# Performance work log

Hardware: AMD Instinct MI355X
Metric: run time of the kernel (lower is better)

The kernel has to match this reference:

```python
import jax, jax.numpy as jnp
import numpy as np

N, E, F_IN, H, T, OUT, ATTR = 20000, 640000, 128, 128, 12, 64, 4


def _glorot(key, shape):
    lim = 1.0 / np.sqrt(shape[0])
    return jax.random.uniform(key, shape, jnp.float32, -lim, lim)


def setup_inputs() -> dict:
    key = jax.random.key(0)
    ks = jax.random.split(key, 48)
    inp = {
        "x": jax.random.normal(ks[0], (N, F_IN, T), jnp.float32),
        "edge_attr": jax.random.uniform(ks[1], (E, ATTR), jnp.float32),
        "edge_index": jax.random.randint(ks[2], (2, E), 0, N, jnp.int32),
    }
    k = 3
    for i, cin in enumerate([F_IN, H]):
        gi = cin + 2 * H
        inp[f"gw{i}"] = _glorot(ks[k], (cin, H)); k += 1
        inp[f"gb{i}"] = jnp.zeros((H,), jnp.float32)
        for g in ["f", "i", "o", "c"]:
            inp[f"w{g}{i}"] = _glorot(ks[k], (gi, H)); k += 1
            inp[f"b{g}{i}"] = jnp.zeros((H,), jnp.float32)
    inp["ow"] = _glorot(ks[k], (H, OUT)); k += 1
    inp["ob"] = jnp.zeros((OUT,), jnp.float32)
    return inp


def _forward(edge_index, x, edge_attr, gw0, gb0, wf0, bf0, wi0, bi0, wo0, bo0, wc0, bc0,
             gw1, gb1, wf1, bf1, wi1, bi1, wo1, bo1, wc1, bc1, ow, ob):
    n = x.shape[0]
    ew = edge_attr[:, -1]
    row, col = edge_index[0], edge_index[1]
    # GCN normalization with self-loops (PyG gcn_norm, improved=False)
    sl = jnp.arange(n, dtype=row.dtype)
    r = jnp.concatenate([row, sl])
    c = jnp.concatenate([col, sl])
    w = jnp.concatenate([ew, jnp.ones((n,), ew.dtype)])
    deg = jax.ops.segment_sum(w, c, num_segments=n)
    dis = jnp.where(deg > 0, 1.0, 0.0) * jax.lax.rsqrt(jnp.where(deg > 0, deg, 1.0))
    norm = dis[r] * w * dis[c]  # [E+N]

    params = [(gw0, gb0, wf0, bf0, wi0, bi0, wo0, bo0, wc0, bc0),
              (gw1, gb1, wf1, bf1, wi1, bi1, wo1, bo1, wc1, bc1)]

    def gcn(xt, gw, gb):
        xw = xt @ gw  # [N,H]
        return jax.ops.segment_sum(norm[:, None] * xw[r], c, num_segments=n) + gb

    def cell(xt, h, cc, p):
        gw, gb, wf, bf, wi, bi, wo, bo, wc, bc = p
        g = jax.nn.sigmoid(gcn(xt, gw, gb))
        zu = jnp.concatenate([xt, g, h], axis=-1)  # [N, in+2H]
        f_t = jax.nn.sigmoid(zu @ wf + bf)
        i_t = jax.nn.sigmoid(zu @ wi + bi)
        o_t = jax.nn.sigmoid(zu @ wo + bo)
        c_t = jnp.tanh(zu @ wc + bc)
        cn = f_t * cc + i_t * c_t
        hn = o_t * jnp.tanh(cn)
        return hn, cn

    z = jnp.zeros((n, H), x.dtype)

    def step(carry, xt):
        inp_t = xt
        new = []
        for i2, p in enumerate(params):
            h, cc = cell(inp_t, carry[i2][0], carry[i2][1], p)
            new.append((h, cc))
            inp_t = h
        return tuple(new), None

    xs = jnp.transpose(x, (2, 0, 1))  # [T, N, F]
    carry, _ = jax.lax.scan(step, tuple((z, z) for _ in params), xs)
    return carry[-1][0] @ ow + ob  # output_activation = Identity


def reference(x, edge_attr, edge_index, gw0, gb0, wf0, bf0, wi0, bi0, wo0, bo0, wc0, bc0,
              gw1, gb1, wf1, bf1, wi1, bi1, wo1, bo1, wc1, bc1, ow, ob):
    return _forward(edge_index, x, edge_attr, gw0, gb0, wf0, bf0, wi0, bi0, wo0, bo0, wc0, bc0,
                    gw1, gb1, wf1, bf1, wi1, bi1, wo1, bo1, wc1, bc1, ow, ob)
```

## Files before the change

kernel.cpp:

```cpp
#include <hip/hip_runtime.h>
#include <hip/hip_bf16.h>

typedef unsigned short u16;
typedef unsigned int   u32;
typedef __attribute__((ext_vector_type(8))) short bf16x8;
typedef __attribute__((ext_vector_type(4))) float f32x4;

#define HDIM 128
#define TSTEPS 12
#define OUTD 64

#define AS1 __attribute__((address_space(1)))
#define AS3 __attribute__((address_space(3)))

__device__ __forceinline__ void glds16(const void* g, void* l) {
  __builtin_amdgcn_global_load_lds((const AS1 u32*)g, (AS3 u32*)l, 16, 0, 0);
}

__device__ __forceinline__ float bflo(u32 u) { return __uint_as_float(u << 16); }
__device__ __forceinline__ float bfhi(u32 u) { return __uint_as_float(u & 0xffff0000u); }
__device__ __forceinline__ u16 f2bf(float x) {
  union { float f; u32 u; } v; v.f = x;
  return (u16)((v.u + 0x7fffu + ((v.u >> 16) & 1u)) >> 16);
}
__device__ __forceinline__ float sigm(float x) { return 1.0f / (1.0f + __expf(-x)); }
__device__ __forceinline__ float tanh_f(float x) { return 1.0f - 2.0f / (__expf(2.0f * x) + 1.0f); }


__global__ void k_init(float* c0, float* c1, u16* h0z, u16* h1z, int* cnt, int* cursor, int N) {
  int i = blockIdx.x * 256 + threadIdx.x;
  int nh = N * HDIM;
  if (i < nh) { c0[i] = 0.f; c1[i] = 0.f; h0z[i] = 0; h1z[i] = 0; }
  if (i < N) { cnt[i] = 1; cursor[i] = 0; }
}

__global__ void k_xpose(const float* __restrict__ x, u16* __restrict__ xb, int N) {
  int i = blockIdx.x * 256 + threadIdx.x;
  if (i >= N * HDIM) return;
  const float* src = x + (size_t)i * 12;
  float4 a = *(const float4*)src;
  float4 b = *(const float4*)(src + 4);
  float4 c = *(const float4*)(src + 8);
  float v[12] = { a.x,a.y,a.z,a.w,b.x,b.y,b.z,b.w,c.x,c.y,c.z,c.w };
#pragma unroll
  for (int t = 0; t < 12; ++t) xb[(size_t)t * N * HDIM + i] = f2bf(v[t]);
}

__global__ void k_cnt(const int* __restrict__ ei, int* cnt, int E) {
  int e = blockIdx.x * 256 + threadIdx.x;
  if (e >= E) return;
  atomicAdd(&cnt[ei[E + e]], 1);
}

__global__ void k_scan(const int* __restrict__ cnt, int* __restrict__ rp, int n) {
  __shared__ int sums[1024];
  int tid = threadIdx.x;
  int chunk = (n + 1023) / 1024;
  int start = tid * chunk;
  int end = start + chunk; if (end > n) end = n;
  int s = 0;
  for (int i = start; i < end; ++i) s += cnt[i];
  sums[tid] = s;
  __syncthreads();
  for (int off = 1; off < 1024; off <<= 1) {
    int v = (tid >= off) ? sums[tid - off] : 0;
    __syncthreads();
    sums[tid] += v;
    __syncthreads();
  }
  int run = (tid == 0) ? 0 : sums[tid - 1];
  for (int i = start; i < end; ++i) { rp[i] = run; run += cnt[i]; }
  if (tid == 1023) rp[n] = sums[1023];
}

__global__ void k_scatter(const int* __restrict__ ei, const float* __restrict__ ea,
                          const int* __restrict__ rp, int* cursor, uint2* ee, int E) {
  int e = blockIdx.x * 256 + threadIdx.x;
  if (e >= E) return;
  int row = ei[e], col = ei[E + e];
  int pos = atomicAdd(&cursor[col], 1);
  int idx = rp[col] + 1 + pos;
  ee[idx] = make_uint2((u32)row << 8, __float_as_uint(ea[e * 4 + 3]));
}

__global__ void k_degcsr(const int* __restrict__ rp, uint2* ee, float* dis, int N) {
  int j = blockIdx.x;
  int lane = threadIdx.x;
  int beg = rp[j], end = rp[j + 1];
  float s = 0.f;
  for (int i = beg + 1 + lane; i < end; i += 64) s += __uint_as_float(ee[i].y);
#pragma unroll
  for (int o = 32; o; o >>= 1) s += __shfl_down(s, o);
  if (lane == 0) {
    dis[j] = rsqrtf(1.0f + s);
    ee[beg] = make_uint2((u32)j << 8, __float_as_uint(1.0f));
  }
}

__global__ void k_enrm(const int* __restrict__ rp, const float* __restrict__ dis,
                       uint2* ee, int N) {
  int j = blockIdx.x;
  int lane = threadIdx.x;
  int beg = rp[j], end = rp[j + 1];
  float dj = dis[j];
  for (int i = beg + lane; i < end; i += 64) {
    uint2 q = ee[i];
    ee[i].y = __float_as_uint(dis[q.x >> 8] * __uint_as_float(q.y) * dj);
  }
}

__global__ void k_wt(const float* __restrict__ src, u16* __restrict__ dst, int K, int J, int ldK) {
  int idx = blockIdx.x * 256 + threadIdx.x;
  if (idx >= K * J) return;
  int k = idx / J, j = idx % J;
  dst[j * ldK + k] = f2bf(src[idx]);
}

__global__ void k_wt4(const float* wf, const float* wi, const float* wo, const float* wc,
                      u16* __restrict__ dst) {
  int idx = blockIdx.x * 256 + threadIdx.x;
  if (idx >= 512 * 384) return;
  int p = idx / 384, k = idx % 384;
  int g = (p >> 4) & 3;
  int hc = (p & 15) | ((p >> 6) << 4);
  const float* w[4] = { wf, wi, wo, wc };
  dst[p * 384 + k] = f2bf(w[g][k * HDIM + hc]);
}

__global__ void k_bias4(const float* bf, const float* bi, const float* bo, const float* bc,
                        float* dst) {
  int p = blockIdx.x * 256 + threadIdx.x;
  if (p >= 512) return;
  int g = (p >> 4) & 3;
  int hc = (p & 15) | ((p >> 6) << 4);
  const float* b[4] = { bf, bi, bo, bc };
  dst[p] = b[g][hc];
}

struct GA {
  const u16* s0; const u16* s1; const u16* s2;
  const u16* wt;
  const float* b4; float* cst; u16* hout;
};
struct GJ { const u16* A; const u16* wt; u16* out; };

__global__ __launch_bounds__(256)
void k_mega(GA ga0, GA ga1, GJ gj, int gjM, int ngate, int M) {
  __shared__ u16 lA[128 * 32];
  __shared__ u16 lB[128 * 32];
  const int y = blockIdx.y;
  const int tid = threadIdx.x;
  const int row0 = blockIdx.x * 128;
  const int wave = tid >> 6, lane = tid & 63;
  const int wm = (wave >> 1) * 64, wn = (wave & 1) * 64;
  const int fr = lane & 15, fk = (lane >> 4) * 8;
  const int lr = tid >> 2, lc = (tid & 3) * 8;
  u16* ldA = lA + wave * 512;
  u16* ldB = lB + wave * 512;
  f32x4 acc[4][4] = {};
  const int fq4 = (lane >> 4) * 4;

  if (y < 4 * ngate) {
    const GA& ga = (y < 4) ? ga0 : ga1;
    const int yy = y & 3;
    const int col0 = yy * 128;
    const u16* segs[3] = { ga.s0, ga.s1, ga.s2 };
    const u16* gb1 = ga.wt + (size_t)(col0 + lr) * 384 + lc;
    const u16* gb2 = gb1 + (size_t)64 * 384;
    const size_t arow1 = (size_t)(row0 + lr) * HDIM + lc;
    const size_t arow2 = arow1 + (size_t)64 * HDIM;

    for (int ks = 0; ks < 12; ++ks) {
      const int k0 = ks * 32;
      const u16* As = segs[ks >> 2];
      const int kk = k0 & 127;
      glds16(As + arow1 + kk, ldA);
      glds16(As + arow2 + kk, ldA + 2048);
      glds16(gb1 + k0, ldB);
      glds16(gb2 + k0, ldB + 2048);
      __syncthreads();
      bf16x8 af[4], bfx[4];
#pragma unroll
      for (int m = 0; m < 4; ++m) af[m]  = *(const bf16x8*)&lA[(wm + m * 16 + fr) * 32 + fk];
#pragma unroll
      for (int n = 0; n < 4; ++n) bfx[n] = *(const bf16x8*)&lB[(wn + n * 16 + fr) * 32 + fk];
#pragma unroll
      for (int m = 0; m < 4; ++m)
#pragma unroll
        for (int n = 0; n < 4; ++n)
          acc[m][n] = __builtin_amdgcn_mfma_f32_16x16x32_bf16(af[m], bfx[n], acc[m][n], 0, 0, 0);
      __syncthreads();
    }

    const int hc = fr | ((yy * 2 + (wave & 1)) << 4);
    const int colbase = col0 + wn + fr;
    const float bb0 = ga.b4[colbase];
    const float bb1 = ga.b4[colbase + 16];
    const float bb2 = ga.b4[colbase + 32];
    const float bb3 = ga.b4[colbase + 48];
#pragma unroll
    for (int m = 0; m < 4; ++m)
#pragma unroll
      for (int i = 0; i < 4; ++i) {
        const int rowg = row0 + wm + m * 16 + fq4 + i;
        if (rowg < M) {
          float f_ = sigm(acc[m][0][i] + bb0);
          float i_ = sigm(acc[m][1][i] + bb1);
          float o_ = sigm(acc[m][2][i] + bb2);
          float cd = tanh_f(acc[m][3][i] + bb3);
          size_t idx = (size_t)rowg * HDIM + hc;
          float cn = f_ * ga.cst[idx] + i_ * cd;
          ga.cst[idx] = cn;
          ga.hout[idx] = f2bf(o_ * tanh_f(cn));
        }
      }
  } else {
    if (row0 >= gjM) return;
    const u16* ga1p = gj.A + (size_t)(row0 + lr) * HDIM + lc;
    const u16* ga2p = ga1p + (size_t)64 * HDIM;
    const u16* gb1p = gj.wt + (size_t)lr * HDIM + lc;
    const u16* gb2p = gb1p + (size_t)64 * HDIM;
    for (int k0 = 0; k0 < 128; k0 += 32) {
      glds16(ga1p + k0, ldA);
      glds16(ga2p + k0, ldA + 2048);
      glds16(gb1p + k0, ldB);
      glds16(gb2p + k0, ldB + 2048);
      __syncthreads();
      bf16x8 af[4], bfx[4];
#pragma unroll
      for (int m = 0; m < 4; ++m) af[m]  = *(const bf16x8*)&lA[(wm + m * 16 + fr) * 32 + fk];
#pragma unroll
      for (int n = 0; n < 4; ++n) bfx[n] = *(const bf16x8*)&lB[(wn + n * 16 + fr) * 32 + fk];
#pragma unroll
      for (int m = 0; m < 4; ++m)
#pragma unroll
        for (int n = 0; n < 4; ++n)
          acc[m][n] = __builtin_amdgcn_mfma_f32_16x16x32_bf16(af[m], bfx[n], acc[m][n], 0, 0, 0);
      __syncthreads();
    }
#pragma unroll
    for (int m = 0; m < 4; ++m)
#pragma unroll
      for (int n = 0; n < 4; ++n) {
        const int colg = wn + n * 16 + fr;
#pragma unroll
        for (int i = 0; i < 4; ++i) {
          const int rowg = row0 + wm + m * 16 + fq4 + i;
          if (rowg < gjM) gj.out[(size_t)rowg * HDIM + colg] = f2bf(acc[m][n][i]);
        }
      }
  }
}

__global__ void k_agg(const u16* __restrict__ xw, const int* __restrict__ rp,
                      const uint2* __restrict__ ee, const float* __restrict__ gb,
                      u16* __restrict__ g, int N) {
  __shared__ uint2 s_e[64];
  const char* xwb = (const char*)xw;
  int bid = blockIdx.x;
  int j = bid % N;
  u32 tbase = (u32)(bid - j) << 8;
  int lane = threadIdx.x;
  int beg = rp[j], end = rp[j + 1];
  const int sl = lane & 31, half = lane >> 5;
  const u32 slB = (u32)sl * 8;
  float a0 = 0.f, a1 = 0.f, a2 = 0.f, a3 = 0.f;
  for (int cb = beg; cb < end; cb += 64) {
    int mc = end - cb; if (mc > 64) mc = 64;
    uint2 q;
    if (lane < mc) { q = ee[cb + lane]; q.x += tbase; }
    else { q.x = tbase; q.y = 0u; }
    s_e[lane] = q;
    __syncthreads();
    int np = (mc + 1) >> 1;
    for (int p = 0; p < np; ++p) {
      uint2 r = s_e[p * 2 + half];
      float w = __uint_as_float(r.y);
      uint2 v = *(const uint2*)(xwb + (r.x + slB));
      a0 += w * bflo(v.x);
      a1 += w * bfhi(v.x);
      a2 += w * bflo(v.y);
      a3 += w * bfhi(v.y);
    }
    __syncthreads();
  }
  a0 += __shfl_xor(a0, 32);
  a1 += __shfl_xor(a1, 32);
  a2 += __shfl_xor(a2, 32);
  a3 += __shfl_xor(a3, 32);
  if (half == 0) {
    float4 bv = *(const float4*)(gb + sl * 4);
    a0 = sigm(a0 + bv.x); a1 = sigm(a1 + bv.y);
    a2 = sigm(a2 + bv.z); a3 = sigm(a3 + bv.w);
    uint2 o;
    o.x = ((u32)f2bf(a1) << 16) | (u32)f2bf(a0);
    o.y = ((u32)f2bf(a3) << 16) | (u32)f2bf(a2);
    *(uint2*)((char*)g + (((size_t)bid) << 8) + slB) = o;
  }
}

__global__ void k_out(const u16* __restrict__ h, const float* __restrict__ ow,
                      const float* __restrict__ ob, float* __restrict__ out, int M) {
  __shared__ float lw[HDIM * OUTD];
  __shared__ float lb[OUTD];
  int tid = threadIdx.x;
  for (int i = tid; i < HDIM * OUTD; i += 256) lw[i] = ow[i];
  if (tid < OUTD) lb[tid] = ob[tid];
  __syncthreads();
  int j = tid & 63;
  int nl = tid >> 6;
  int n = blockIdx.x * 4 + nl;
  if (n >= M) return;
  const u16* hr = h + (size_t)n * HDIM;
  float s = lb[j];
#pragma unroll 4
  for (int k = 0; k < HDIM; ++k) s += bflo((u32)hr[k] << 0 ? (u32)hr[k] : (u32)hr[k]) * 0.f + __uint_as_float(((u32)hr[k]) << 16) * lw[k * OUTD + j];
  out[(size_t)n * OUTD + j] = s;
}

extern "C" void kernel_launch(void* const* d_in, const int* in_sizes, int n_in,
                              void* d_out, int out_size, void* d_ws, size_t ws_size,
                              hipStream_t stream) {
  const float* x  = (const float*)d_in[0];
  const float* ea = (const float*)d_in[1];
  const int*   ei = (const int*)d_in[2];
  const float* gw[2] = { (const float*)d_in[3],  (const float*)d_in[13] };
  const float* gb[2] = { (const float*)d_in[4],  (const float*)d_in[14] };
  const float* wg[2][4] = {
    { (const float*)d_in[5],  (const float*)d_in[7],  (const float*)d_in[9],  (const float*)d_in[11] },
    { (const float*)d_in[15], (const float*)d_in[17], (const float*)d_in[19], (const float*)d_in[21] } };
  const float* bg[2][4] = {
    { (const float*)d_in[6],  (const float*)d_in[8],  (const float*)d_in[10], (const float*)d_in[12] },
    { (const float*)d_in[16], (const float*)d_in[18], (const float*)d_in[20], (const float*)d_in[22] } };
  const float* ow = (const float*)d_in[23];
  const float* ob = (const float*)d_in[24];
  float* out = (float*)d_out;

  const int N = in_sizes[0] / (HDIM * TSTEPS);
  const int E = in_sizes[2] / 2;
  const int nh = N * HDIM;
  const int tnh = TSTEPS * nh;

  size_t off = 0;
  auto alloc = [&](size_t bytes) -> void* {
    void* p = (char*)d_ws + off;
    off += (bytes + 255) & ~(size_t)255;
    return p;
  };
  u16* xb     = (u16*)alloc((size_t)tnh * 2);
  u16* xw_all = (u16*)alloc((size_t)tnh * 2);
  u16* g0_all = (u16*)alloc((size_t)tnh * 2);
  u16* H0[3] = { (u16*)alloc((size_t)nh * 2), (u16*)alloc((size_t)nh * 2), (u16*)alloc((size_t)nh * 2) };
  u16* H1[2] = { (u16*)alloc((size_t)nh * 2), (u16*)alloc((size_t)nh * 2) };
  u16* g1buf = (u16*)alloc((size_t)nh * 2);
  u16* xw1[2] = { (u16*)alloc((size_t)nh * 2), (u16*)alloc((size_t)nh * 2) };
  float* cst[2] = { (float*)alloc((size_t)nh * 4), (float*)alloc((size_t)nh * 4) };
  float* dis   = (float*)alloc((size_t)N * 4);
  int* cnt     = (int*)alloc((size_t)N * 4);
  int* cursor  = (int*)alloc((size_t)N * 4);
  int* rp      = (int*)alloc((size_t)(N + 1) * 4);
  uint2* ee    = (uint2*)alloc((size_t)(E + N) * 8);
  u16* gwT[2] = { (u16*)alloc(HDIM * HDIM * 2), (u16*)alloc(HDIM * HDIM * 2) };
  u16* w4T[2] = { (u16*)alloc(512 * 384 * 2),   (u16*)alloc(512 * 384 * 2) };
  float* b4[2] = { (float*)alloc(512 * 4), (float*)alloc(512 * 4) };
  alloc(32768);

  k_init<<<(nh + 255) / 256, 256, 0, stream>>>(cst[0], cst[1], H0[2], H1[1], cnt, cursor, N);
  k_xpose<<<(nh + 255) / 256, 256, 0, stream>>>(x, xb, N);
  k_cnt<<<(E + 255) / 256, 256, 0, stream>>>(ei, cnt, E);
  k_scan<<<1, 1024, 0, stream>>>(cnt, rp, N);
  k_scatter<<<(E + 255) / 256, 256, 0, stream>>>(ei, ea, rp, cursor, ee, E);
  k_degcsr<<<N, 64, 0, stream>>>(rp, ee, dis, N);
  k_enrm<<<N, 64, 0, stream>>>(rp, dis, ee, N);
  for (int l = 0; l < 2; ++l) {
    k_wt<<<(HDIM * HDIM + 255) / 256, 256, 0, stream>>>(gw[l], gwT[l], HDIM, HDIM, HDIM);
    k_wt4<<<(512 * 384 + 255) / 256, 256, 0, stream>>>(wg[l][0], wg[l][1], wg[l][2], wg[l][3], w4T[l]);
    k_bias4<<<2, 256, 0, stream>>>(bg[l][0], bg[l][1], bg[l][2], bg[l][3], b4[l]);
  }

  const int nb = (N + 127) / 128;
  GA zga = { xb, xb, xb, w4T[0], b4[0], cst[0], H0[0] };
  GJ zgj = { xb, gwT[0], xw_all };

  {
    int Mb = tnh / HDIM;
    GJ gj = { xb, gwT[0], xw_all };
    k_mega<<<dim3((Mb + 127) / 128, 1), 256, 0, stream>>>(zga, zga, gj, Mb, 0, N);
  }
  k_agg<<<TSTEPS * N, 64, 0, stream>>>(xw_all, rp, ee, gb[0], g0_all, N);

  {
    GA a0 = { xb, g0_all, H0[2], w4T[0], b4[0], cst[0], H0[0] };
    k_mega<<<dim3(nb, 4), 256, 0, stream>>>(a0, a0, zgj, N, 1, N);
  }
  {
    GA a0 = { xb + (size_t)nh, g0_all + (size_t)nh, H0[0], w4T[0], b4[0], cst[0], H0[1] };
    GJ gj = { H0[0], gwT[1], xw1[0] };
    k_mega<<<dim3(nb, 5), 256, 0, stream>>>(a0, a0, gj, N, 1, N);
  }

  for (int t = 0; t < TSTEPS; ++t) {
    k_agg<<<N, 64, 0, stream>>>(xw1[t & 1], rp, ee, gb[1], g1buf, N);
    GA a0 = { H0[t % 3], g1buf, H1[(t + 1) & 1], w4T[1], b4[1], cst[1], H1[t & 1] };
    int ngate = 1, hasg = 0;
    GA a1 = a0;
    GJ gj = zgj;
    if (t + 2 < TSTEPS) {
      a1 = GA{ xb + (size_t)(t + 2) * nh, g0_all + (size_t)(t + 2) * nh, H0[(t + 1) % 3],
               w4T[0], b4[0], cst[0], H0[(t + 2) % 3] };
      ngate = 2;
    }
    if (t + 1 < TSTEPS) {
      gj = GJ{ H0[(t + 1) % 3], gwT[1], xw1[(t + 1) & 1] };
      hasg = 1;
    }
    k_mega<<<dim3(nb, 4 * ngate + hasg), 256, 0, stream>>>(a0, a1, gj, N, ngate, N);
  }
  k_out<<<(N + 3) / 4, 256, 0, stream>>>(H1[1], ow, ob, out, N);
}
```

Baseline: 1.439 ms.

## Run layers sequentially with node-major all-timestep GCN aggregation

Restructures the schedule so that layer 0 runs for all timesteps first, then layer 1. Each layer's GCN linear step and neighbour aggregation now run once over all 12 timesteps, using a node-major layout so one CSR traversal per node gathers every timestep's features in a single contiguous row. This replaces the per-step aggregation launches for layer 1 and the fused mega-kernel with separate gate kernels. It removes the repeated edge-list traversals and many small launches. In exchange it keeps all layer-0 hidden states in memory, reuses buffers, and drops the overlap of layer-0 and layer-1 work within a single launch.

```diff
diff --git a/kernel.cpp b/kernel.cpp
--- a/kernel.cpp
+++ b/kernel.cpp
@@ -9,9 +9,13 @@
 #define HDIM 128
 #define TSTEPS 12
 #define OUTD 64
+#define NTMAJ 1536
+#define NTB   3072
 
 #define AS1 __attribute__((address_space(1)))
 #define AS3 __attribute__((address_space(3)))
+
+struct u32x3 { u32 x, y, z; };
 
 __device__ __forceinline__ void glds16(const void* g, void* l) {
   __builtin_amdgcn_global_load_lds((const AS1 u32*)g, (AS3 u32*)l, 16, 0, 0);
@@ -27,11 +31,14 @@
 __device__ __forceinline__ float tanh_f(float x) { return 1.0f - 2.0f / (__expf(2.0f * x) + 1.0f); }
 
 
-__global__ void k_init(float* c0, float* c1, u16* h0z, u16* h1z, int* cnt, int* cursor, int N) {
+__global__ void k_init(int* cnt, int* cursor, int N) {
   int i = blockIdx.x * 256 + threadIdx.x;
-  int nh = N * HDIM;
-  if (i < nh) { c0[i] = 0.f; c1[i] = 0.f; h0z[i] = 0; h1z[i] = 0; }
   if (i < N) { cnt[i] = 1; cursor[i] = 0; }
+}
+
+__global__ void k_zero(u32* p, int n) {
+  int i = blockIdx.x * 256 + threadIdx.x;
+  if (i < n) p[i] = 0;
 }
 
 __global__ void k_xpose(const float* __restrict__ x, u16* __restrict__ xb, int N) {
@@ -80,7 +87,7 @@
   int row = ei[e], col = ei[E + e];
   int pos = atomicAdd(&cursor[col], 1);
   int idx = rp[col] + 1 + pos;
-  ee[idx] = make_uint2((u32)row << 8, __float_as_uint(ea[e * 4 + 3]));
+  ee[idx] = make_uint2((u32)row * NTB, __float_as_uint(ea[e * 4 + 3]));
 }
 
 __global__ void k_degcsr(const int* __restrict__ rp, uint2* ee, float* dis, int N) {
@@ -93,7 +100,7 @@
   for (int o = 32; o; o >>= 1) s += __shfl_down(s, o);
   if (lane == 0) {
     dis[j] = rsqrtf(1.0f + s);
-    ee[beg] = make_uint2((u32)j << 8, __float_as_uint(1.0f));
+    ee[beg] = make_uint2((u32)j * NTB, __float_as_uint(1.0f));
   }
 }
 
@@ -105,7 +112,7 @@
   float dj = dis[j];
   for (int i = beg + lane; i < end; i += 64) {
     uint2 q = ee[i];
-    ee[i].y = __float_as_uint(dis[q.x >> 8] * __uint_as_float(q.y) * dj);
+    ee[i].y = __float_as_uint(dis[q.x / NTB] * __uint_as_float(q.y) * dj);
   }
 }
 
@@ -137,18 +144,12 @@
   dst[p] = b[g][hc];
 }
 
-struct GA {
-  const u16* s0; const u16* s1; const u16* s2;
-  const u16* wt;
-  const float* b4; float* cst; u16* hout;
-};
-struct GJ { const u16* A; const u16* wt; u16* out; };
-
 __global__ __launch_bounds__(256)
-void k_mega(GA ga0, GA ga1, GJ gj, int gjM, int ngate, int M) {
+void k_gcnlin(const u16* __restrict__ A, const u16* __restrict__ wt,
+              u16* __restrict__ out, int N, int nh) {
   __shared__ u16 lA[128 * 32];
   __shared__ u16 lB[128 * 32];
-  const int y = blockIdx.y;
+  const int t = blockIdx.y;
   const int tid = threadIdx.x;
   const int row0 = blockIdx.x * 128;
   const int wave = tid >> 6, lane = tid & 63;
@@ -157,146 +158,154 @@
   const int lr = tid >> 2, lc = (tid & 3) * 8;
   u16* ldA = lA + wave * 512;
   u16* ldB = lB + wave * 512;
+  const u16* ga1 = A + (size_t)t * nh + (size_t)(row0 + lr) * HDIM + lc;
+  const u16* ga2 = ga1 + (size_t)64 * HDIM;
+  const u16* gb1 = wt + (size_t)lr * HDIM + lc;
+  const u16* gb2 = gb1 + (size_t)64 * HDIM;
+
   f32x4 acc[4][4] = {};
+  for (int k0 = 0; k0 < 128; k0 += 32) {
+    glds16(ga1 + k0, ldA);
+    glds16(ga2 + k0, ldA + 2048);
+    glds16(gb1 + k0, ldB);
+    glds16(gb2 + k0, ldB + 2048);
+    __syncthreads();
+    bf16x8 af[4], bfx[4];
+#pragma unroll
+    for (int m = 0; m < 4; ++m) af[m]  = *(const bf16x8*)&lA[(wm + m * 16 + fr) * 32 + fk];
+#pragma unroll
+    for (int n = 0; n < 4; ++n) bfx[n] = *(const bf16x8*)&lB[(wn + n * 16 + fr) * 32 + fk];
+#pragma unroll
+    for (int m = 0; m < 4; ++m)
+#pragma unroll
+      for (int n = 0; n < 4; ++n)
+        acc[m][n] = __builtin_amdgcn_mfma_f32_16x16x32_bf16(af[m], bfx[n], acc[m][n], 0, 0, 0);
+    __syncthreads();
+  }
   const int fq4 = (lane >> 4) * 4;
-
-  if (y < 4 * ngate) {
-    const GA& ga = (y < 4) ? ga0 : ga1;
-    const int yy = y & 3;
-    const int col0 = yy * 128;
-    const u16* segs[3] = { ga.s0, ga.s1, ga.s2 };
-    const u16* gb1 = ga.wt + (size_t)(col0 + lr) * 384 + lc;
-    const u16* gb2 = gb1 + (size_t)64 * 384;
-    const size_t arow1 = (size_t)(row0 + lr) * HDIM + lc;
-    const size_t arow2 = arow1 + (size_t)64 * HDIM;
-
-    for (int ks = 0; ks < 12; ++ks) {
-      const int k0 = ks * 32;
-      const u16* As = segs[ks >> 2];
-      const int kk = k0 & 127;
-      glds16(As + arow1 + kk, ldA);
-      glds16(As + arow2 + kk, ldA + 2048);
-      glds16(gb1 + k0, ldB);
-      glds16(gb2 + k0, ldB + 2048);
-      __syncthreads();
-      bf16x8 af[4], bfx[4];
-#pragma unroll
-      for (int m = 0; m < 4; ++m) af[m]  = *(const bf16x8*)&lA[(wm + m * 16 + fr) * 32 + fk];
-#pragma unroll
-      for (int n = 0; n < 4; ++n) bfx[n] = *(const bf16x8*)&lB[(wn + n * 16 + fr) * 32 + fk];
-#pragma unroll
-      for (int m = 0; m < 4; ++m)
-#pragma unroll
-        for (int n = 0; n < 4; ++n)
-          acc[m][n] = __builtin_amdgcn_mfma_f32_16x16x32_bf16(af[m], bfx[n], acc[m][n], 0, 0, 0);
-      __syncthreads();
-    }
-
-    const int hc = fr | ((yy * 2 + (wave & 1)) << 4);
-    const int colbase = col0 + wn + fr;
-    const float bb0 = ga.b4[colbase];
-    const float bb1 = ga.b4[colbase + 16];
-    const float bb2 = ga.b4[colbase + 32];
-    const float bb3 = ga.b4[colbase + 48];
-#pragma unroll
-    for (int m = 0; m < 4; ++m)
+#pragma unroll
+  for (int m = 0; m < 4; ++m)
+#pragma unroll
+    for (int n = 0; n < 4; ++n) {
+      const int colg = wn + n * 16 + fr;
 #pragma unroll
       for (int i = 0; i < 4; ++i) {
         const int rowg = row0 + wm + m * 16 + fq4 + i;
-        if (rowg < M) {
-          float f_ = sigm(acc[m][0][i] + bb0);
-          float i_ = sigm(acc[m][1][i] + bb1);
-          float o_ = sigm(acc[m][2][i] + bb2);
-          float cd = tanh_f(acc[m][3][i] + bb3);
-          size_t idx = (size_t)rowg * HDIM + hc;
-          float cn = f_ * ga.cst[idx] + i_ * cd;
-          ga.cst[idx] = cn;
-          ga.hout[idx] = f2bf(o_ * tanh_f(cn));
-        }
+        if (rowg < N) out[(size_t)rowg * NTMAJ + t * HDIM + colg] = f2bf(acc[m][n][i]);
       }
-  } else {
-    if (row0 >= gjM) return;
-    const u16* ga1p = gj.A + (size_t)(row0 + lr) * HDIM + lc;
-    const u16* ga2p = ga1p + (size_t)64 * HDIM;
-    const u16* gb1p = gj.wt + (size_t)lr * HDIM + lc;
-    const u16* gb2p = gb1p + (size_t)64 * HDIM;
-    for (int k0 = 0; k0 < 128; k0 += 32) {
-      glds16(ga1p + k0, ldA);
-      glds16(ga2p + k0, ldA + 2048);
-      glds16(gb1p + k0, ldB);
-      glds16(gb2p + k0, ldB + 2048);
-      __syncthreads();
-      bf16x8 af[4], bfx[4];
-#pragma unroll
-      for (int m = 0; m < 4; ++m) af[m]  = *(const bf16x8*)&lA[(wm + m * 16 + fr) * 32 + fk];
-#pragma unroll
-      for (int n = 0; n < 4; ++n) bfx[n] = *(const bf16x8*)&lB[(wn + n * 16 + fr) * 32 + fk];
-#pragma unroll
-      for (int m = 0; m < 4; ++m)
-#pragma unroll
-        for (int n = 0; n < 4; ++n)
-          acc[m][n] = __builtin_amdgcn_mfma_f32_16x16x32_bf16(af[m], bfx[n], acc[m][n], 0, 0, 0);
-      __syncthreads();
     }
+}
+
+__global__ __launch_bounds__(256)
+void k_gate3(const u16* __restrict__ p0, u32 st0,
+             const u16* __restrict__ p1, u32 st1,
+             const u16* __restrict__ p2, u32 st2,
+             const u16* __restrict__ wt, const float* __restrict__ b4p,
+             float* __restrict__ cst, u16* __restrict__ hout, int M) {
+  __shared__ u16 lA[128 * 32];
+  __shared__ u16 lB[128 * 32];
+  const int col0 = blockIdx.y * 128;
+  const int tid = threadIdx.x;
+  const int row0 = blockIdx.x * 128;
+  const int wave = tid >> 6, lane = tid & 63;
+  const int wm = (wave >> 1) * 64, wn = (wave & 1) * 64;
+  const int fr = lane & 15, fk = (lane >> 4) * 8;
+  const int lr = tid >> 2, lc = (tid & 3) * 8;
+  u16* ldA = lA + wave * 512;
+  u16* ldB = lB + wave * 512;
+  const u16* a1[3]; const u16* a2[3];
+  a1[0] = p0 + (size_t)(row0 + lr) * st0 + lc;  a2[0] = a1[0] + (size_t)64 * st0;
+  a1[1] = p1 + (size_t)(row0 + lr) * st1 + lc;  a2[1] = a1[1] + (size_t)64 * st1;
+  a1[2] = p2 + (size_t)(row0 + lr) * st2 + lc;  a2[2] = a1[2] + (size_t)64 * st2;
+  const u16* gb1 = wt + (size_t)(col0 + lr) * 384 + lc;
+  const u16* gb2 = gb1 + (size_t)64 * 384;
+
+  f32x4 acc[4][4] = {};
+#pragma unroll
+  for (int ks = 0; ks < 12; ++ks) {
+    const int seg = ks >> 2;
+    const int kk = (ks & 3) * 32;
+    glds16(a1[seg] + kk, ldA);
+    glds16(a2[seg] + kk, ldA + 2048);
+    glds16(gb1 + ks * 32, ldB);
+    glds16(gb2 + ks * 32, ldB + 2048);
+    __syncthreads();
+    bf16x8 af[4], bfx[4];
+#pragma unroll
+    for (int m = 0; m < 4; ++m) af[m]  = *(const bf16x8*)&lA[(wm + m * 16 + fr) * 32 + fk];
+#pragma unroll
+    for (int n = 0; n < 4; ++n) bfx[n] = *(const bf16x8*)&lB[(wn + n * 16 + fr) * 32 + fk];
 #pragma unroll
     for (int m = 0; m < 4; ++m)
 #pragma unroll
-      for (int n = 0; n < 4; ++n) {
-        const int colg = wn + n * 16 + fr;
-#pragma unroll
-        for (int i = 0; i < 4; ++i) {
-          const int rowg = row0 + wm + m * 16 + fq4 + i;
-          if (rowg < gjM) gj.out[(size_t)rowg * HDIM + colg] = f2bf(acc[m][n][i]);
-        }
+      for (int n = 0; n < 4; ++n)
+        acc[m][n] = __builtin_amdgcn_mfma_f32_16x16x32_bf16(af[m], bfx[n], acc[m][n], 0, 0, 0);
+    __syncthreads();
+  }
+
+  const int fq4 = (lane >> 4) * 4;
+  const int hc = fr | ((blockIdx.y * 2 + (wave & 1)) << 4);
+  const int colbase = col0 + wn + fr;
+  const float bb0 = b4p[colbase];
+  const float bb1 = b4p[colbase + 16];
+  const float bb2 = b4p[colbase + 32];
+  const float bb3 = b4p[colbase + 48];
+#pragma unroll
+  for (int m = 0; m < 4; ++m)
+#pragma unroll
+    for (int i = 0; i < 4; ++i) {
+      const int rowg = row0 + wm + m * 16 + fq4 + i;
+      if (rowg < M) {
+        float f_ = sigm(acc[m][0][i] + bb0);
+        float i_ = sigm(acc[m][1][i] + bb1);
+        float o_ = sigm(acc[m][2][i] + bb2);
+        float cd = tanh_f(acc[m][3][i] + bb3);
+        size_t idx = (size_t)rowg * HDIM + hc;
+        float cn = f_ * cst[idx] + i_ * cd;
+        cst[idx] = cn;
+        hout[idx] = f2bf(o_ * tanh_f(cn));
       }
-  }
-}
-
-__global__ void k_agg(const u16* __restrict__ xw, const int* __restrict__ rp,
-                      const uint2* __restrict__ ee, const float* __restrict__ gb,
-                      u16* __restrict__ g, int N) {
-  __shared__ uint2 s_e[64];
-  const char* xwb = (const char*)xw;
-  int bid = blockIdx.x;
-  int j = bid % N;
-  u32 tbase = (u32)(bid - j) << 8;
-  int lane = threadIdx.x;
-  int beg = rp[j], end = rp[j + 1];
-  const int sl = lane & 31, half = lane >> 5;
-  const u32 slB = (u32)sl * 8;
-  float a0 = 0.f, a1 = 0.f, a2 = 0.f, a3 = 0.f;
-  for (int cb = beg; cb < end; cb += 64) {
-    int mc = end - cb; if (mc > 64) mc = 64;
-    uint2 q;
-    if (lane < mc) { q = ee[cb + lane]; q.x += tbase; }
-    else { q.x = tbase; q.y = 0u; }
-    s_e[lane] = q;
-    __syncthreads();
-    int np = (mc + 1) >> 1;
-    for (int p = 0; p < np; ++p) {
-      uint2 r = s_e[p * 2 + half];
+    }
+}
+
+__global__ void k_aggB(const u16* __restrict__ xw, const int* __restrict__ rp,
+                       const uint2* __restrict__ ee, const float* __restrict__ gbias,
+                       u16* __restrict__ g, int N) {
+  __shared__ uint2 s_e[256];
+  __shared__ float s_b[128];
+  const int j = blockIdx.x;
+  const int tid = threadIdx.x;
+  if (tid < 128) s_b[tid] = gbias[tid];
+  const int beg = rp[j], end = rp[j + 1];
+  const char* base = (const char*)xw;
+  const u32 myoff = (u32)tid * 12;
+  float a0 = 0.f, a1 = 0.f, a2 = 0.f, a3 = 0.f, a4 = 0.f, a5 = 0.f;
+  for (int cb = beg; cb < end; cb += 256) {
+    int mc = end - cb; if (mc > 256) mc = 256;
+    if (tid < mc) s_e[tid] = ee[cb + tid];
+    __syncthreads();
+    for (int e = 0; e < mc; ++e) {
+      uint2 r = s_e[e];
       float w = __uint_as_float(r.y);
-      uint2 v = *(const uint2*)(xwb + (r.x + slB));
-      a0 += w * bflo(v.x);
-      a1 += w * bfhi(v.x);
-      a2 += w * bflo(v.y);
-      a3 += w * bfhi(v.y);
+      u32x3 v = *(const u32x3*)(base + (r.x + myoff));
+      a0 += w * bflo(v.x); a1 += w * bfhi(v.x);
+      a2 += w * bflo(v.y); a3 += w * bfhi(v.y);
+      a4 += w * bflo(v.z); a5 += w * bfhi(v.z);
     }
     __syncthreads();
   }
-  a0 += __shfl_xor(a0, 32);
-  a1 += __shfl_xor(a1, 32);
-  a2 += __shfl_xor(a2, 32);
-  a3 += __shfl_xor(a3, 32);
-  if (half == 0) {
-    float4 bv = *(const float4*)(gb + sl * 4);
-    a0 = sigm(a0 + bv.x); a1 = sigm(a1 + bv.y);
-    a2 = sigm(a2 + bv.z); a3 = sigm(a3 + bv.w);
-    uint2 o;
-    o.x = ((u32)f2bf(a1) << 16) | (u32)f2bf(a0);
-    o.y = ((u32)f2bf(a3) << 16) | (u32)f2bf(a2);
-    *(uint2*)((char*)g + (((size_t)bid) << 8) + slB) = o;
-  }
+  const int e0 = tid * 6;
+  float r0 = sigm(a0 + s_b[e0 & 127]);
+  float r1 = sigm(a1 + s_b[(e0 + 1) & 127]);
+  float r2 = sigm(a2 + s_b[(e0 + 2) & 127]);
+  float r3 = sigm(a3 + s_b[(e0 + 3) & 127]);
+  float r4 = sigm(a4 + s_b[(e0 + 4) & 127]);
+  float r5 = sigm(a5 + s_b[(e0 + 5) & 127]);
+  u32x3 o;
+  o.x = ((u32)f2bf(r1) << 16) | (u32)f2bf(r0);
+  o.y = ((u32)f2bf(r3) << 16) | (u32)f2bf(r2);
+  o.z = ((u32)f2bf(r5) << 16) | (u32)f2bf(r4);
+  *(u32x3*)((char*)g + ((size_t)j * NTB + myoff)) = o;
 }
 
 __global__ void k_out(const u16* __restrict__ h, const float* __restrict__ ow,
@@ -314,7 +323,7 @@
   const u16* hr = h + (size_t)n * HDIM;
   float s = lb[j];
 #pragma unroll 4
-  for (int k = 0; k < HDIM; ++k) s += bflo((u32)hr[k] << 0 ? (u32)hr[k] : (u32)hr[k]) * 0.f + __uint_as_float(((u32)hr[k]) << 16) * lw[k * OUTD + j];
+  for (int k = 0; k < HDIM; ++k) s += __uint_as_float(((u32)hr[k]) << 16) * lw[k * OUTD + j];
   out[(size_t)n * OUTD + j] = s;
 }
 
@@ -348,24 +357,24 @@
     return p;
   };
   u16* xb     = (u16*)alloc((size_t)tnh * 2);
-  u16* xw_all = (u16*)alloc((size_t)tnh * 2);
-  u16* g0_all = (u16*)alloc((size_t)tnh * 2);
-  u16* H0[3] = { (u16*)alloc((size_t)nh * 2), (u16*)alloc((size_t)nh * 2), (u16*)alloc((size_t)nh * 2) };
-  u16* H1[2] = { (u16*)alloc((size_t)nh * 2), (u16*)alloc((size_t)nh * 2) };
-  u16* g1buf = (u16*)alloc((size_t)nh * 2);
-  u16* xw1[2] = { (u16*)alloc((size_t)nh * 2), (u16*)alloc((size_t)nh * 2) };
-  float* cst[2] = { (float*)alloc((size_t)nh * 4), (float*)alloc((size_t)nh * 4) };
-  float* dis   = (float*)alloc((size_t)N * 4);
-  int* cnt     = (int*)alloc((size_t)N * 4);
-  int* cursor  = (int*)alloc((size_t)N * 4);
-  int* rp      = (int*)alloc((size_t)(N + 1) * 4);
-  uint2* ee    = (uint2*)alloc((size_t)(E + N) * 8);
+  u16* g_nm   = (u16*)alloc((size_t)tnh * 2);
+  u16* h0_all = (u16*)alloc((size_t)(TSTEPS + 1) * nh * 2);
+  float* cst  = (float*)alloc((size_t)nh * 4);
+  uint2* ee   = (uint2*)alloc((size_t)(E + N) * 8);
+  float* dis  = (float*)alloc((size_t)N * 4);
+  int* cnt    = (int*)alloc((size_t)N * 4);
+  int* cursor = (int*)alloc((size_t)N * 4);
+  int* rp     = (int*)alloc((size_t)(N + 1) * 4);
   u16* gwT[2] = { (u16*)alloc(HDIM * HDIM * 2), (u16*)alloc(HDIM * HDIM * 2) };
   u16* w4T[2] = { (u16*)alloc(512 * 384 * 2),   (u16*)alloc(512 * 384 * 2) };
   float* b4[2] = { (float*)alloc(512 * 4), (float*)alloc(512 * 4) };
-  alloc(32768);
-
-  k_init<<<(nh + 255) / 256, 256, 0, stream>>>(cst[0], cst[1], H0[2], H1[1], cnt, cursor, N);
+  alloc(131072);
+
+  u16* XW0 = h0_all;
+  u16* XW1 = xb;
+  u16* H1[2] = { xb, xb + (size_t)nh };
+
+  k_init<<<(N + 255) / 256, 256, 0, stream>>>(cnt, cursor, N);
   k_xpose<<<(nh + 255) / 256, 256, 0, stream>>>(x, xb, N);
   k_cnt<<<(E + 255) / 256, 256, 0, stream>>>(ei, cnt, E);
   k_scan<<<1, 1024, 0, stream>>>(cnt, rp, N);
@@ -379,42 +388,30 @@
   }
 
   const int nb = (N + 127) / 128;
-  GA zga = { xb, xb, xb, w4T[0], b4[0], cst[0], H0[0] };
-  GJ zgj = { xb, gwT[0], xw_all };
-
-  {
-    int Mb = tnh / HDIM;
-    GJ gj = { xb, gwT[0], xw_all };
-    k_mega<<<dim3((Mb + 127) / 128, 1), 256, 0, stream>>>(zga, zga, gj, Mb, 0, N);
-  }
-  k_agg<<<TSTEPS * N, 64, 0, stream>>>(xw_all, rp, ee, gb[0], g0_all, N);
-
-  {
-    GA a0 = { xb, g0_all, H0[2], w4T[0], b4[0], cst[0], H0[0] };
-    k_mega<<<dim3(nb, 4), 256, 0, stream>>>(a0, a0, zgj, N, 1, N);
-  }
-  {
-    GA a0 = { xb + (size_t)nh, g0_all + (size_t)nh, H0[0], w4T[0], b4[0], cst[0], H0[1] };
-    GJ gj = { H0[0], gwT[1], xw1[0] };
-    k_mega<<<dim3(nb, 5), 256, 0, stream>>>(a0, a0, gj, N, 1, N);
-  }
-
-  for (int t = 0; t < TSTEPS; ++t) {
-    k_agg<<<N, 64, 0, stream>>>(xw1[t & 1], rp, ee, gb[1], g1buf, N);
-    GA a0 = { H0[t % 3], g1buf, H1[(t + 1) & 1], w4T[1], b4[1], cst[1], H1[t & 1] };
-    int ngate = 1, hasg = 0;
-    GA a1 = a0;
-    GJ gj = zgj;
-    if (t + 2 < TSTEPS) {
-      a1 = GA{ xb + (size_t)(t + 2) * nh, g0_all + (size_t)(t + 2) * nh, H0[(t + 1) % 3],
-               w4T[0], b4[0], cst[0], H0[(t + 2) % 3] };
-      ngate = 2;
-    }
-    if (t + 1 < TSTEPS) {
-      gj = GJ{ H0[(t + 1) % 3], gwT[1], xw1[(t + 1) & 1] };
-      hasg = 1;
-    }
-    k_mega<<<dim3(nb, 4 * ngate + hasg), 256, 0, stream>>>(a0, a1, gj, N, ngate, N);
-  }
+
+  k_gcnlin<<<dim3(nb, TSTEPS), 256, 0, stream>>>(xb, gwT[0], XW0, N, nh);
+  k_aggB<<<N, 256, 0, stream>>>(XW0, rp, ee, gb[0], g_nm, N);
+  k_zero<<<(nh / 2 + 255) / 256, 256, 0, stream>>>((u32*)h0_all, nh / 2);
+  k_zero<<<(nh + 255) / 256, 256, 0, stream>>>((u32*)cst, nh);
+
+  for (int t = 0; t < TSTEPS; ++t)
+    k_gate3<<<dim3(nb, 4), 256, 0, stream>>>(
+        xb + (size_t)t * nh, HDIM,
+        g_nm + (size_t)t * HDIM, NTMAJ,
+        h0_all + (size_t)t * nh, HDIM,
+        w4T[0], b4[0], cst, h0_all + (size_t)(t + 1) * nh, N);
+
+  k_gcnlin<<<dim3(nb, TSTEPS), 256, 0, stream>>>(h0_all + nh, gwT[1], XW1, N, nh);
+  k_aggB<<<N, 256, 0, stream>>>(XW1, rp, ee, gb[1], g_nm, N);
+  k_zero<<<(nh / 2 + 255) / 256, 256, 0, stream>>>((u32*)H1[1], nh / 2);
+  k_zero<<<(nh + 255) / 256, 256, 0, stream>>>((u32*)cst, nh);
+
+  for (int t = 0; t < TSTEPS; ++t)
+    k_gate3<<<dim3(nb, 4), 256, 0, stream>>>(
+        h0_all + (size_t)(t + 1) * nh, HDIM,
+        g_nm + (size_t)t * HDIM, NTMAJ,
+        H1[(t + 1) & 1], HDIM,
+        w4T[1], b4[1], cst, H1[t & 1], N);
+
   k_out<<<(N + 3) / 4, 256, 0, stream>>>(H1[1], ow, ob, out, N);
 }
```

After: 1.605 ms. 1.12x slower.
